# Optimization experiments

Measured on AMD Instinct MI355X. Metric: run time of the kernel, lower is better.

## Reference

```python
import jax, jax.numpy as jnp
import numpy as np

B, DIM, HH, WW = 8, 512, 64, 64
HEADS, DH = 8, 64
INNER = HEADS * DH
EPS = 1e-5  # ChanLayerNorm2D eps


def _chan_norm(x, g, b):
    # channel-wise layernorm over axis 1 (biased variance, like torch.var(unbiased=False))
    m = jnp.mean(x, axis=1, keepdims=True)
    v = jnp.mean((x - m) ** 2, axis=1, keepdims=True)
    return (x - m) / jnp.sqrt(v + EPS) * g + b


def _l2norm(x):
    # F.normalize(dim=1), eps=1e-12
    n = jnp.sqrt(jnp.sum(x * x, axis=1, keepdims=True))
    return x / jnp.maximum(n, 1e-12)


def setup_inputs() -> dict:
    key = jax.random.key(0)
    ks = jax.random.split(key, 10)
    sc = 1.0 / np.sqrt(DIM)
    return {
        "context": jax.random.normal(ks[0], (B, DIM, HH, WW), jnp.float32),
        "query_source": jax.random.normal(ks[1], (B, DIM, HH, WW), jnp.float32),
        "ctx_g": jnp.ones((1, DIM, 1, 1), jnp.float32),
        "ctx_b": jnp.zeros((1, DIM, 1, 1), jnp.float32),
        "qs_g": jnp.ones((1, DIM, 1, 1), jnp.float32),
        "qs_b": jnp.zeros((1, DIM, 1, 1), jnp.float32),
        "w_q": jax.random.normal(ks[2], (INNER, DIM), jnp.float32) * sc,
        "w_kv": jax.random.normal(ks[3], (2 * INNER, DIM), jnp.float32) * sc,
        "w_out": jax.random.normal(ks[4], (DIM, INNER), jnp.float32) * (1.0 / np.sqrt(INNER)),
        "gamma": jax.random.normal(ks[5], (1,), jnp.float32) * 0.5,
    }


def reference(context, query_source, ctx_g, ctx_b, qs_g, qs_b, w_q, w_kv, w_out, gamma):
    b, c, height, width = query_source.shape
    kh = int(height ** 0.5)  # default height_top_k
    kw = int(width ** 0.5)   # default width_top_k

    ctx = _chan_norm(context, ctx_g, ctx_b)
    qs = _chan_norm(query_source, qs_g, qs_b)

    # 1x1 convs as GEMMs
    kv = jnp.einsum('oi,bihw->bohw', w_kv, ctx)
    k, v = jnp.split(kv, 2, axis=1)
    q = jnp.einsum('oi,bihw->bohw', w_q, qs)

    def fold(t):  # b (h c) H W -> (b h) c H W
        return t.reshape(b, HEADS, DH, height, width).reshape(b * HEADS, DH, height, width)

    q, k, v = fold(q), fold(k), fold(v)
    q, k = _l2norm(q), _l2norm(k)

    # dual pruning (kh < height and kw < width here)
    q_abs = jnp.abs(q)
    k_abs = jnp.abs(k)
    q_probe = jnp.sum(q_abs, axis=(2, 3))            # (bh, c)

    # height selection
    k_height = jnp.sum(k_abs, axis=3)                # (bh, c, H)
    score_r = jnp.einsum('bc,bch->bh', q_probe, k_height)
    _, idx_h = jax.lax.top_k(score_r, kh)            # (bh, kh)
    k = jnp.take_along_axis(k, idx_h[:, None, :, None], axis=2)
    v = jnp.take_along_axis(v, idx_h[:, None, :, None], axis=2)

    # width selection (scores use pre-height-gather k_abs, as in original)
    k_width = jnp.sum(k_abs, axis=2)                 # (bh, c, W)
    score_c = jnp.einsum('bc,bcw->bw', q_probe, k_width)
    _, idx_w = jax.lax.top_k(score_c, kw)            # (bh, kw)
    k = jnp.take_along_axis(k, idx_w[:, None, None, :], axis=3)
    v = jnp.take_along_axis(v, idx_w[:, None, None, :], axis=3)

    def flat(t):  # (bh) d h w -> (bh) (h w) d
        bh, d, h_, w_ = t.shape
        return t.transpose(0, 2, 3, 1).reshape(bh, h_ * w_, d)

    qf, kf, vf = flat(q), flat(k), flat(v)
    attn = jax.nn.softmax(jnp.einsum('bid,bjd->bij', qf, kf), axis=-1)
    out = jnp.einsum('bij,bjd->bid', attn, vf)       # (bh, H*W, d)

    out = out.reshape(b, HEADS, height, width, DH).transpose(0, 1, 4, 2, 3)
    out = out.reshape(b, INNER, height, width)
    out = jnp.einsum('oi,bihw->bohw', w_out, out)
    return gamma[0] * out + qs
```

## Files before the change

kernel.cpp:

```cpp
#include <hip/hip_runtime.h>
#include <math.h>

#define HW 4096
#define DIM 512

typedef __attribute__((ext_vector_type(8))) short short8;
typedef __attribute__((ext_vector_type(4))) float f32x4;

__device__ inline unsigned short f2bf(float f) {
    unsigned int u = __float_as_uint(f);
    u += 0x7fff + ((u >> 16) & 1);
    return (unsigned short)(u >> 16);
}
__device__ inline float bf2f(unsigned short h) {
    return __uint_as_float(((unsigned int)h) << 16);
}
__device__ inline unsigned pack2(float a, float b) {
    return (unsigned)f2bf(a) | ((unsigned)f2bf(b) << 16);
}

__device__ inline void gld16(const void* g, void* lds) {
    __builtin_amdgcn_global_load_lds(
        (const __attribute__((address_space(1))) unsigned int*)g,
        (__attribute__((address_space(3))) unsigned int*)lds, 16, 0, 0);
}

__global__ void prep_weights(const float* __restrict__ w_q, const float* __restrict__ w_kv,
                             const float* __restrict__ w_out,
                             const float* __restrict__ ctx_g, const float* __restrict__ ctx_b,
                             const float* __restrict__ qs_g, const float* __restrict__ qs_b,
                             unsigned short* __restrict__ wq_b, unsigned short* __restrict__ wk_b,
                             unsigned short* __restrict__ wo_b, float* __restrict__ wv_g,
                             float* __restrict__ Avec, float* __restrict__ Cvec)
{
    int blk = blockIdx.x;
    int widx = blk >> 9;
    int o = blk & 511;
    int tid = threadIdx.x;
    const float *src, *g = nullptr, *beta = nullptr;
    if (widx == 0)      { src = w_q  + (size_t)o * DIM; g = qs_g;  beta = qs_b; }
    else if (widx == 1) { src = w_kv + (size_t)o * DIM; g = ctx_g; beta = ctx_b; }
    else if (widx == 2) { src = w_kv + (size_t)(512 + o) * DIM; g = ctx_g; beta = ctx_b; }
    else                { src = w_out + (size_t)o * DIM; }
    float a = 0.f, c = 0.f;
    for (int i = tid; i < DIM; i += 256) {
        float w = src[i];
        if (widx == 3) { wo_b[(size_t)o * DIM + i] = f2bf(w); continue; }
        float wg = w * g[i];
        if (widx == 0)      wq_b[(size_t)o * DIM + i] = f2bf(wg);
        else if (widx == 1) wk_b[(size_t)o * DIM + i] = f2bf(wg);
        else                wv_g[(size_t)o * DIM + i] = wg;
        a += wg; c += w * beta[i];
    }
    if (widx == 3) return;
    __shared__ float sa[256], sc[256];
    sa[tid] = a; sc[tid] = c;
    __syncthreads();
    for (int s = 128; s > 0; s >>= 1) {
        if (tid < s) { sa[tid] += sa[tid + s]; sc[tid] += sc[tid + s]; }
        __syncthreads();
    }
    if (tid == 0) { Avec[widx * 512 + o] = sa[0]; Cvec[widx * 512 + o] = sc[0]; }
}

__global__ __launch_bounds__(256) void conv_stats(
    const float* __restrict__ ctx, const float* __restrict__ qs,
    unsigned short* __restrict__ ctx_t, unsigned short* __restrict__ qs_t,
    float* __restrict__ ctx_m, float* __restrict__ ctx_r,
    float* __restrict__ qs_m, float* __restrict__ qs_r)
{
    int which = blockIdx.z;
    int b = blockIdx.y;
    int p0 = blockIdx.x * 64;
    const float* X = (which ? qs : ctx) + (size_t)b * DIM * HW;
    unsigned short* Xt = (which ? qs_t : ctx_t) + (size_t)b * HW * DIM;
    int tid = threadIdx.x;
    int p = tid & 63;
    int q4 = tid >> 6;
    const float* col = X + p0 + p;

    __shared__ uint4 tile[64 * 32];
    __shared__ float sbuf[256], ssbuf[256];

    float s = 0.f, ss = 0.f;
    for (int chunk = 0; chunk < 2; chunk++) {
        for (int si = 0; si < 8; si++) {
            int cgl = q4 * 8 + si;
            int c = chunk * 256 + cgl * 8;
            float v[8];
#pragma unroll
            for (int j = 0; j < 8; j++) {
                v[j] = col[(size_t)(c + j) * HW];
                s += v[j]; ss = fmaf(v[j], v[j], ss);
            }
            uint4 pk;
            pk.x = pack2(v[0], v[1]);
            pk.y = pack2(v[2], v[3]);
            pk.z = pack2(v[4], v[5]);
            pk.w = pack2(v[6], v[7]);
            tile[p * 32 + (cgl ^ (p & 15))] = pk;
        }
        __syncthreads();
        int pr = tid >> 2, c2 = tid & 3;
        unsigned short* orow = Xt + (size_t)(p0 + pr) * 512 + chunk * 256;
#pragma unroll
        for (int si = 0; si < 8; si++) {
            int cgl = c2 + si * 4;
            uint4 d = tile[pr * 32 + (cgl ^ (pr & 15))];
            *(uint4*)(orow + cgl * 8) = d;
        }
        __syncthreads();
    }

    sbuf[tid] = s; ssbuf[tid] = ss;
    __syncthreads();
    if (tid < 64) {
        float st  = sbuf[tid] + sbuf[tid + 64] + sbuf[tid + 128] + sbuf[tid + 192];
        float sst = ssbuf[tid] + ssbuf[tid + 64] + ssbuf[tid + 128] + ssbuf[tid + 192];
        float m = st * (1.0f / DIM);
        float var = sst * (1.0f / DIM) - m * m;
        float r = 1.0f / sqrtf(var + 1e-5f);
        int pix = b * HW + p0 + tid;
        if (which == 0) { ctx_m[pix] = m; ctx_r[pix] = r; }
        else            { qs_m[pix]  = m; qs_r[pix]  = r; }
    }
}

template<int MODE>
__global__ __launch_bounds__(256) void gemm_mfma(
    const unsigned short* __restrict__ Wb, const unsigned short* __restrict__ Xt,
    float* __restrict__ Y, unsigned short* __restrict__ Ybf,
    const float* __restrict__ mean, const float* __restrict__ rstd,
    const float* __restrict__ Arow, const float* __restrict__ Crow,
    float* __restrict__ probe,
    const float* __restrict__ qsrc, const float* __restrict__ g,
    const float* __restrict__ beta, const float* __restrict__ gammaPtr)
{
    int b = blockIdx.z;
    int n0 = blockIdx.x * 128;
    int m0 = blockIdx.y * 128;
    const unsigned short* Xb = Xt + (size_t)b * HW * DIM;
    __shared__ uint4 AsBuf[512];
    __shared__ uint4 BsBuf[512];
    unsigned short* As = (unsigned short*)AsBuf;
    unsigned short* Bs = (unsigned short*)BsBuf;
    int tid = threadIdx.x;
    int lane = tid & 63;
    int wave = tid >> 6;
    int wbase = tid & 192;
    int wm = (wave >> 1) * 64;
    int wn = (wave & 1) * 64;
    int quad = lane >> 4;
    int l16 = lane & 15;

    int r0 = tid >> 2, c0 = (tid & 3) * 8;
    const unsigned short* pA0 = Wb + (size_t)(m0 + r0) * DIM + c0;
    const unsigned short* pA1 = Wb + (size_t)(m0 + 64 + r0) * DIM + c0;
    const unsigned short* pB0 = Xb + (size_t)(n0 + r0) * DIM + c0;
    const unsigned short* pB1 = Xb + (size_t)(n0 + 64 + r0) * DIM + c0;

    f32x4 acc[4][4];
#pragma unroll
    for (int i = 0; i < 4; i++)
#pragma unroll
        for (int j = 0; j < 4; j++) acc[i][j] = (f32x4){0.f, 0.f, 0.f, 0.f};

    for (int kt = 0; kt < 16; kt++) {
        gld16(pA0, AsBuf + wbase);
        gld16(pA1, AsBuf + 256 + wbase);
        gld16(pB0, BsBuf + wbase);
        gld16(pB1, BsBuf + 256 + wbase);
        pA0 += 32; pA1 += 32; pB0 += 32; pB1 += 32;
        __syncthreads();
        short8 af[4], bfr[4];
#pragma unroll
        for (int i = 0; i < 4; i++)
            af[i] = *(const short8*)(As + (wm + i * 16 + l16) * 32 + quad * 8);
#pragma unroll
        for (int j = 0; j < 4; j++)
            bfr[j] = *(const short8*)(Bs + (wn + j * 16 + l16) * 32 + quad * 8);
#pragma unroll
        for (int i = 0; i < 4; i++)
#pragma unroll
            for (int j = 0; j < 4; j++)
                acc[i][j] = __builtin_amdgcn_mfma_f32_16x16x32_bf16(af[i], bfr[j], acc[i][j], 0, 0, 0);
        __syncthreads();
    }

    if (MODE < 2) {
        float pa[4][4] = {};
#pragma unroll
        for (int j = 0; j < 4; j++) {
            int n = n0 + wn + j * 16 + l16;
            int pix = b * HW + n;
            float mn = mean[pix], rs = rstd[pix];
            float y[4][4];
            float s2 = 0.f;
#pragma unroll
            for (int i = 0; i < 4; i++) {
                int mb = m0 + wm + i * 16 + quad * 4;
#pragma unroll
                for (int r = 0; r < 4; r++) {
                    float v = rs * (acc[i][j][r] - mn * Arow[mb + r]) + Crow[mb + r];
                    y[i][r] = v;
                    s2 = fmaf(v, v, s2);
                }
            }
            s2 += __shfl_xor(s2, 16, 64);
            s2 += __shfl_xor(s2, 32, 64);
            float inv = 1.0f / fmaxf(sqrtf(s2), 1e-12f);
            unsigned short* orow = Ybf + (size_t)(b * HW + n) * 512 + m0 + wm + quad * 4;
#pragma unroll
            for (int i = 0; i < 4; i++) {
                float v0 = y[i][0] * inv, v1 = y[i][1] * inv;
                float v2 = y[i][2] * inv, v3 = y[i][3] * inv;
                uint2 pk; pk.x = pack2(v0, v1); pk.y = pack2(v2, v3);
                *(uint2*)(orow + i * 16) = pk;
                pa[i][0] += fabsf(v0); pa[i][1] += fabsf(v1);
                pa[i][2] += fabsf(v2); pa[i][3] += fabsf(v3);
            }
        }
#pragma unroll
        for (int i = 0; i < 4; i++)
#pragma unroll
            for (int r = 0; r < 4; r++) {
                float v = pa[i][r];
                v += __shfl_xor(v, 1, 64);
                v += __shfl_xor(v, 2, 64);
                v += __shfl_xor(v, 4, 64);
                v += __shfl_xor(v, 8, 64);
                pa[i][r] = v;
            }
        if (l16 == 0) {
#pragma unroll
            for (int i = 0; i < 4; i++)
#pragma unroll
                for (int r = 0; r < 4; r++) {
                    int m = m0 + wm + i * 16 + quad * 4 + r;
                    if (MODE == 0) atomicAdd(&probe[b * 512 + m], pa[i][r]);
                    else atomicAdd(&probe[(size_t)(b * 512 + m) * 64 + ((n0 + wn) >> 6)], pa[i][r]);
                }
        }
    } else {
        float* Yb = Y + (size_t)b * DIM * HW;
        float gamma = gammaPtr[0];
        const float* qb = qsrc + (size_t)b * DIM * HW;
#pragma unroll
        for (int j = 0; j < 4; j++) {
            int n = n0 + wn + j * 16 + l16;
            int pix = b * HW + n;
            float mn = mean[pix], rs = rstd[pix];
#pragma unroll
            for (int i = 0; i < 4; i++) {
                int mb = m0 + wm + i * 16 + quad * 4;
#pragma unroll
                for (int r = 0; r < 4; r++) {
                    int m = mb + r;
                    float qn = (qb[(size_t)m * HW + n] - mn) * rs * g[m] + beta[m];
                    Yb[(size_t)m * HW + n] = gamma * acc[i][j][r] + qn;
                }
            }
        }
    }
}

__global__ __launch_bounds__(256) void kws_kernel(const unsigned short* __restrict__ kbf,
                                                  float* __restrict__ kws)
{
    int blk = blockIdx.x;
    int b = blk >> 6, w = blk & 63;
    int tid = threadIdx.x;
    int c8 = tid & 63;
    int hq = tid >> 6;
    float a[8] = {};
    for (int hh = 0; hh < 16; hh++) {
        const unsigned short* row = kbf + ((size_t)(b * HW + (hq * 16 + hh) * 64 + w)) * 512 + c8 * 8;
        uint4 pk = *(const uint4*)row;
        const unsigned short* u = (const unsigned short*)&pk;
#pragma unroll
        for (int j = 0; j < 8; j++) a[j] += fabsf(bf2f(u[j]));
    }
    __shared__ float red[512 * 4];
#pragma unroll
    for (int j = 0; j < 8; j++) red[(c8 * 8 + j) * 4 + hq] = a[j];
    __syncthreads();
    if (tid < 256) {
        int c = tid;
        float v0 = red[c * 4] + red[c * 4 + 1] + red[c * 4 + 2] + red[c * 4 + 3];
        int c2 = tid + 256;
        float v1 = red[c2 * 4] + red[c2 * 4 + 1] + red[c2 * 4 + 2] + red[c2 * 4 + 3];
        kws[(size_t)(b * 512 + c) * 64 + w] = v0;
        kws[(size_t)(b * 512 + c2) * 64 + w] = v1;
    }
}

__global__ void score_topk(const float* __restrict__ qp, const float* __restrict__ khs,
                           const float* __restrict__ kws, int* __restrict__ idx_h, int* __restrict__ idx_w)
{
    int bh = blockIdx.x;
    int lane = threadIdx.x;
    float sr = 0.f, sc = 0.f;
    for (int c = 0; c < 64; c++) {
        float q = qp[bh * 64 + c];
        sr = fmaf(q, khs[(size_t)(bh * 64 + c) * 64 + lane], sr);
        sc = fmaf(q, kws[(size_t)(bh * 64 + c) * 64 + lane], sc);
    }
    float v = sr;
    for (int it = 0; it < 8; it++) {
        float bv = v; int bi = lane;
        for (int off = 1; off < 64; off <<= 1) {
            float ov = __shfl_xor(bv, off, 64);
            int oi = __shfl_xor(bi, off, 64);
            if (ov > bv || (ov == bv && oi < bi)) { bv = ov; bi = oi; }
        }
        if (lane == 0) idx_h[bh * 8 + it] = bi;
        if (lane == bi) v = -INFINITY;
    }
    v = sc;
    for (int it = 0; it < 8; it++) {
        float bv = v; int bi = lane;
        for (int off = 1; off < 64; off <<= 1) {
            float ov = __shfl_xor(bv, off, 64);
            int oi = __shfl_xor(bi, off, 64);
            if (ov > bv || (ov == bv && oi < bi)) { bv = ov; bi = oi; }
        }
        if (lane == 0) idx_w[bh * 8 + it] = bi;
        if (lane == bi) v = -INFINITY;
    }
}

__global__ void gather_kv(const unsigned short* __restrict__ kbf, const unsigned short* __restrict__ ctx_t,
                          const float* __restrict__ wv_g, const float* __restrict__ Av, const float* __restrict__ Cv,
                          const float* __restrict__ ctx_m, const float* __restrict__ ctx_r,
                          const int* __restrict__ idx_h, const int* __restrict__ idx_w,
                          unsigned short* __restrict__ kg, unsigned short* __restrict__ vgt)
{
    int blk = blockIdx.x;
    int bh = blk >> 6, j = blk & 63;
    int h = idx_h[bh * 8 + (j >> 3)];
    int w = idx_w[bh * 8 + (j & 7)];
    int p = h * 64 + w;
    int b = bh >> 3, head = bh & 7;
    int d = threadIdx.x;
    kg[(size_t)blk * 64 + d] = kbf[(size_t)(b * HW + p) * 512 + head * 64 + d];
    __shared__ float cx[DIM];
    const unsigned short* crow = ctx_t + (size_t)(b * HW + p) * 512;
    short8 cv = ((const short8*)crow)[d];
#pragma unroll
    for (int u = 0; u < 8; u++) cx[d * 8 + u] = bf2f((unsigned short)cv[u]);
    __syncthreads();
    int o = head * 64 + d;
    const float* wrow = wv_g + (size_t)o * DIM;
    float acc = 0.f;
    for (int i = 0; i < DIM; i++) acc = fmaf(wrow[i], cx[i], acc);
    int pix = b * HW + p;
    float v = ctx_r[pix] * (acc - ctx_m[pix] * Av[o]) + Cv[o];
    vgt[((size_t)bh * 64 + d) * 64 + j] = f2bf(v);
}

#define PROW 72
__global__ __launch_bounds__(256) void attn_mfma(
    const unsigned short* __restrict__ qbf, const unsigned short* __restrict__ kg,
    const unsigned short* __restrict__ vgt, unsigned short* __restrict__ abuf)
{
    int bh = blockIdx.y;
    int b = bh >> 3, head = bh & 7;
    int tid = threadIdx.x;
    int lane = tid & 63, wave = tid >> 6;
    int g = lane >> 4, l16 = lane & 15;
    int p0 = blockIdx.x * 256 + wave * 64;

    __shared__ unsigned short Plds[4][64 * PROW];
    unsigned short* P = Plds[wave];

    const unsigned short* kgb = kg + (size_t)bh * 4096;
    const unsigned short* vtb = vgt + (size_t)bh * 4096;
    const unsigned short* qb = qbf + (size_t)(b * HW) * 512 + head * 64;

    short8 Qf[4][2];
#pragma unroll
    for (int j = 0; j < 4; j++)
#pragma unroll
        for (int t = 0; t < 2; t++)
            Qf[j][t] = *(const short8*)(qb + (size_t)(p0 + j * 16 + l16) * 512 + t * 32 + g * 8);

    f32x4 S[4][4];
#pragma unroll
    for (int i = 0; i < 4; i++)
#pragma unroll
        for (int j = 0; j < 4; j++) S[i][j] = (f32x4){0.f, 0.f, 0.f, 0.f};
#pragma unroll
    for (int t = 0; t < 2; t++) {
        short8 Kf[4];
#pragma unroll
        for (int i = 0; i < 4; i++)
            Kf[i] = *(const short8*)(kgb + (i * 16 + l16) * 64 + t * 32 + g * 8);
#pragma unroll
        for (int i = 0; i < 4; i++)
#pragma unroll
            for (int j = 0; j < 4; j++)
                S[i][j] = __builtin_amdgcn_mfma_f32_16x16x32_bf16(Kf[i], Qf[j][t], S[i][j], 0, 0, 0);
    }

    float inv[4];
#pragma unroll
    for (int j = 0; j < 4; j++) {
        float e[4][4];
        float s = 0.f;
#pragma unroll
        for (int i = 0; i < 4; i++)
#pragma unroll
            for (int r = 0; r < 4; r++) { e[i][r] = __expf(S[i][j][r]); s += e[i][r]; }
        s += __shfl_xor(s, 16, 64);
        s += __shfl_xor(s, 32, 64);
        inv[j] = 1.0f / s;
        int row = j * 16 + l16;
#pragma unroll
        for (int i = 0; i < 4; i++) {
            uint2 pk;
            pk.x = pack2(e[i][0], e[i][1]);
            pk.y = pack2(e[i][2], e[i][3]);
            *(uint2*)(P + row * PROW + i * 16 + g * 4) = pk;
        }
    }

    f32x4 O[4][4];
#pragma unroll
    for (int i = 0; i < 4; i++)
#pragma unroll
        for (int j = 0; j < 4; j++) O[i][j] = (f32x4){0.f, 0.f, 0.f, 0.f};
#pragma unroll
    for (int t = 0; t < 2; t++) {
        short8 Vf[4], Pf[4];
#pragma unroll
        for (int i = 0; i < 4; i++)
            Vf[i] = *(const short8*)(vtb + (i * 16 + l16) * 64 + t * 32 + g * 8);
#pragma unroll
        for (int j = 0; j < 4; j++)
            Pf[j] = *(const short8*)(P + (j * 16 + l16) * PROW + t * 32 + g * 8);
#pragma unroll
        for (int i = 0; i < 4; i++)
#pragma unroll
            for (int j = 0; j < 4; j++)
                O[i][j] = __builtin_amdgcn_mfma_f32_16x16x32_bf16(Vf[i], Pf[j], O[i][j], 0, 0, 0);
    }

    unsigned short* ob = abuf + (size_t)(b * HW) * 512 + head * 64;
#pragma unroll
    for (int j = 0; j < 4; j++) {
        int p = p0 + j * 16 + l16;
#pragma unroll
        for (int i = 0; i < 4; i++) {
            uint2 pk;
            pk.x = pack2(O[i][j][0] * inv[j], O[i][j][1] * inv[j]);
            pk.y = pack2(O[i][j][2] * inv[j], O[i][j][3] * inv[j]);
            *(uint2*)(ob + (size_t)p * 512 + i * 16 + g * 4) = pk;
        }
    }
}

extern "C" void kernel_launch(void* const* d_in, const int* in_sizes, int n_in,
                              void* d_out, int out_size, void* d_ws, size_t ws_size,
                              hipStream_t stream)
{
    (void)in_sizes; (void)n_in; (void)out_size; (void)ws_size;
    const float* ctx   = (const float*)d_in[0];
    const float* qs    = (const float*)d_in[1];
    const float* ctx_g = (const float*)d_in[2];
    const float* ctx_b = (const float*)d_in[3];
    const float* qs_g  = (const float*)d_in[4];
    const float* qs_b  = (const float*)d_in[5];
    const float* w_q   = (const float*)d_in[6];
    const float* w_kv  = (const float*)d_in[7];
    const float* w_out = (const float*)d_in[8];
    const float* gamma = (const float*)d_in[9];
    float* out = (float*)d_out;

    char* base = (char*)d_ws;
    unsigned short* ctx_t = (unsigned short*)base;
    unsigned short* abuf  = ctx_t;
    unsigned short* qs_t  = (unsigned short*)(base + ((size_t)32 << 20));
    unsigned short* kbf   = qs_t;
    unsigned short* qbf   = (unsigned short*)(base + ((size_t)64 << 20));
    char* tail = base + ((size_t)96 << 20);
    unsigned short* wq_b = (unsigned short*)tail;
    unsigned short* wk_b = wq_b + 262144;
    unsigned short* wo_b = wk_b + 262144;
    float* wv_g  = (float*)(wo_b + 262144);
    float* Avec  = wv_g + 262144;
    float* Cvec  = Avec + 1536;
    float* ctx_m = Cvec + 1536;
    float* ctx_r = ctx_m + 32768;
    float* qs_m  = ctx_r + 32768;
    float* qs_r  = qs_m + 32768;
    float* qp    = qs_r + 32768;
    float* khs   = qp + 4096;
    float* kws   = khs + 262144;
    int*   idxh  = (int*)(kws + 262144);
    int*   idxw  = idxh + 512;
    unsigned short* kg  = (unsigned short*)(idxw + 512);
    unsigned short* vgt = kg + 262144;

    hipMemsetAsync(qp, 0, 4096 * sizeof(float), stream);
    hipMemsetAsync(khs, 0, 262144 * sizeof(float), stream);

    prep_weights<<<2048, 256, 0, stream>>>(w_q, w_kv, w_out, ctx_g, ctx_b, qs_g, qs_b,
                                           wq_b, wk_b, wo_b, wv_g, Avec, Cvec);
    conv_stats<<<dim3(64, 8, 2), 256, 0, stream>>>(ctx, qs, ctx_t, qs_t,
                                                   ctx_m, ctx_r, qs_m, qs_r);
    gemm_mfma<0><<<dim3(32, 4, 8), 256, 0, stream>>>(wq_b, qs_t, nullptr, qbf, qs_m, qs_r,
                                                     Avec, Cvec, qp, nullptr, nullptr, nullptr, nullptr);
    gemm_mfma<1><<<dim3(32, 4, 8), 256, 0, stream>>>(wk_b, ctx_t, nullptr, kbf, ctx_m, ctx_r,
                                                     Avec + 512, Cvec + 512, khs, nullptr, nullptr, nullptr, nullptr);
    kws_kernel<<<512, 256, 0, stream>>>(kbf, kws);
    score_topk<<<64, 64, 0, stream>>>(qp, khs, kws, idxh, idxw);
    gather_kv<<<4096, 64, 0, stream>>>(kbf, ctx_t, wv_g, Avec + 1024, Cvec + 1024,
                                       ctx_m, ctx_r, idxh, idxw, kg, vgt);
    attn_mfma<<<dim3(16, 64), 256, 0, stream>>>(qbf, kg, vgt, abuf);
    gemm_mfma<2><<<dim3(32, 4, 8), 256, 0, stream>>>(wo_b, abuf, out, nullptr, qs_m, qs_r,
                                                     nullptr, nullptr, nullptr, qs, qs_g, qs_b, gamma);
}
```

Measured before the change: 450.5 us.

## Split conv_stats across channel slices with atomic stat accumulation

The transpose-and-stats kernel now tiles over 32-channel by 512-pixel blocks, giving 2048 blocks instead of 1024. It loads float4 rows coalesced along pixels and transposes through a padded LDS tile into the bf16 channel-last layout. Per-pixel sum and sum-of-squares are accumulated across channel slices with global atomics, and a new finalize kernel turns them into mean and rstd. This aims to improve load coalescing and parallelism on a memory-bound pass, at the cost of an extra memset, an extra launch, and atomic traffic.

```diff
diff --git a/kernel.cpp b/kernel.cpp
--- a/kernel.cpp
+++ b/kernel.cpp
@@ -66,64 +66,96 @@
 __global__ __launch_bounds__(256) void conv_stats(
     const float* __restrict__ ctx, const float* __restrict__ qs,
     unsigned short* __restrict__ ctx_t, unsigned short* __restrict__ qs_t,
-    float* __restrict__ ctx_m, float* __restrict__ ctx_r,
-    float* __restrict__ qs_m, float* __restrict__ qs_r)
-{
-    int which = blockIdx.z;
-    int b = blockIdx.y;
-    int p0 = blockIdx.x * 64;
+    float* __restrict__ Sacc, float* __restrict__ Qacc)
+{
+    int id = blockIdx.x;
+    int pstrip = id & 7;
+    int cs = (id >> 3) & 15;
+    int b = (id >> 7) & 7;
+    int which = id >> 10;
+
     const float* X = (which ? qs : ctx) + (size_t)b * DIM * HW;
     unsigned short* Xt = (which ? qs_t : ctx_t) + (size_t)b * HW * DIM;
     int tid = threadIdx.x;
-    int p = tid & 63;
-    int q4 = tid >> 6;
-    const float* col = X + p0 + p;
-
-    __shared__ uint4 tile[64 * 32];
-    __shared__ float sbuf[256], ssbuf[256];
-
-    float s = 0.f, ss = 0.f;
-    for (int chunk = 0; chunk < 2; chunk++) {
-        for (int si = 0; si < 8; si++) {
-            int cgl = q4 * 8 + si;
-            int c = chunk * 256 + cgl * 8;
-            float v[8];
-#pragma unroll
-            for (int j = 0; j < 8; j++) {
-                v[j] = col[(size_t)(c + j) * HW];
-                s += v[j]; ss = fmaf(v[j], v[j], ss);
-            }
-            uint4 pk;
-            pk.x = pack2(v[0], v[1]);
-            pk.y = pack2(v[2], v[3]);
-            pk.z = pack2(v[4], v[5]);
-            pk.w = pack2(v[6], v[7]);
-            tile[p * 32 + (cgl ^ (p & 15))] = pk;
-        }
-        __syncthreads();
-        int pr = tid >> 2, c2 = tid & 3;
-        unsigned short* orow = Xt + (size_t)(p0 + pr) * 512 + chunk * 256;
-#pragma unroll
-        for (int si = 0; si < 8; si++) {
-            int cgl = c2 + si * 4;
-            uint4 d = tile[pr * 32 + (cgl ^ (pr & 15))];
-            *(uint4*)(orow + cgl * 8) = d;
-        }
-        __syncthreads();
-    }
-
-    sbuf[tid] = s; ssbuf[tid] = ss;
+    int p0 = pstrip * 512;
+    int c0 = cs * 32;
+
+    __shared__ unsigned short tile[32 * 514];
+    __shared__ float4 sT[128], qT[128];
+
+    int par = tid >> 7;
+    int t7 = tid & 127;
+    int pxl = t7 * 4;
+    const float* src = X + (size_t)(c0 + par) * HW + p0 + pxl;
+
+    float4 s4 = {0.f, 0.f, 0.f, 0.f};
+    float4 q4 = {0.f, 0.f, 0.f, 0.f};
+
+#pragma unroll
+    for (int i = 0; i < 16; i++) {
+        int c = 2 * i + par;
+        float4 v = *(const float4*)(src + (size_t)(2 * i) * HW);
+        s4.x += v.x; s4.y += v.y; s4.z += v.z; s4.w += v.w;
+        q4.x = fmaf(v.x, v.x, q4.x);
+        q4.y = fmaf(v.y, v.y, q4.y);
+        q4.z = fmaf(v.z, v.z, q4.z);
+        q4.w = fmaf(v.w, v.w, q4.w);
+        uint2 pk;
+        pk.x = pack2(v.x, v.y);
+        pk.y = pack2(v.z, v.w);
+        *(uint2*)(tile + c * 514 + pxl) = pk;
+    }
+
+    if (par) { sT[t7] = s4; qT[t7] = q4; }
     __syncthreads();
-    if (tid < 64) {
-        float st  = sbuf[tid] + sbuf[tid + 64] + sbuf[tid + 128] + sbuf[tid + 192];
-        float sst = ssbuf[tid] + ssbuf[tid + 64] + ssbuf[tid + 128] + ssbuf[tid + 192];
-        float m = st * (1.0f / DIM);
-        float var = sst * (1.0f / DIM) - m * m;
-        float r = 1.0f / sqrtf(var + 1e-5f);
-        int pix = b * HW + p0 + tid;
-        if (which == 0) { ctx_m[pix] = m; ctx_r[pix] = r; }
-        else            { qs_m[pix]  = m; qs_r[pix]  = r; }
-    }
+    if (!par) {
+        float4 o = sT[t7];
+        s4.x += o.x; s4.y += o.y; s4.z += o.z; s4.w += o.w;
+        o = qT[t7];
+        q4.x += o.x; q4.y += o.y; q4.z += o.z; q4.w += o.w;
+        int slot = which * 32768 + b * 4096 + p0 + pxl;
+        atomicAdd(&Sacc[slot + 0], s4.x);
+        atomicAdd(&Sacc[slot + 1], s4.y);
+        atomicAdd(&Sacc[slot + 2], s4.z);
+        atomicAdd(&Sacc[slot + 3], s4.w);
+        atomicAdd(&Qacc[slot + 0], q4.x);
+        atomicAdd(&Qacc[slot + 1], q4.y);
+        atomicAdd(&Qacc[slot + 2], q4.z);
+        atomicAdd(&Qacc[slot + 3], q4.w);
+    }
+
+    int cg = tid & 3;
+    int pxw = tid >> 2;
+#pragma unroll
+    for (int r = 0; r < 8; r++) {
+        int px = pxw + 64 * r;
+        const unsigned short* tr = tile + cg * 8 * 514 + px;
+        unsigned short u0 = tr[0 * 514], u1 = tr[1 * 514];
+        unsigned short u2 = tr[2 * 514], u3 = tr[3 * 514];
+        unsigned short u4 = tr[4 * 514], u5 = tr[5 * 514];
+        unsigned short u6 = tr[6 * 514], u7 = tr[7 * 514];
+        uint4 o;
+        o.x = (unsigned)u0 | ((unsigned)u1 << 16);
+        o.y = (unsigned)u2 | ((unsigned)u3 << 16);
+        o.z = (unsigned)u4 | ((unsigned)u5 << 16);
+        o.w = (unsigned)u6 | ((unsigned)u7 << 16);
+        *(uint4*)(Xt + (size_t)(p0 + px) * 512 + c0 + cg * 8) = o;
+    }
+}
+
+__global__ __launch_bounds__(256) void finalize_stats(
+    const float* __restrict__ Sacc, const float* __restrict__ Qacc,
+    float* __restrict__ ctx_m, float* __restrict__ ctx_r,
+    float* __restrict__ qs_m, float* __restrict__ qs_r)
+{
+    int i = blockIdx.x * 256 + threadIdx.x;
+    float s = Sacc[i], q = Qacc[i];
+    float m = s * (1.0f / DIM);
+    float var = q * (1.0f / DIM) - m * m;
+    float r = 1.0f / sqrtf(var + 1e-5f);
+    int pix = i & 32767;
+    if (i < 32768) { ctx_m[pix] = m; ctx_r[pix] = r; }
+    else           { qs_m[pix]  = m; qs_r[pix]  = r; }
 }
 
 template<int MODE>
@@ -500,14 +532,17 @@
     int*   idxw  = idxh + 512;
     unsigned short* kg  = (unsigned short*)(idxw + 512);
     unsigned short* vgt = kg + 262144;
+    float* Sacc = (float*)(vgt + 262144);
+    float* Qacc = Sacc + 65536;
 
     hipMemsetAsync(qp, 0, 4096 * sizeof(float), stream);
     hipMemsetAsync(khs, 0, 262144 * sizeof(float), stream);
+    hipMemsetAsync(Sacc, 0, 131072 * sizeof(float), stream);
 
     prep_weights<<<2048, 256, 0, stream>>>(w_q, w_kv, w_out, ctx_g, ctx_b, qs_g, qs_b,
                                            wq_b, wk_b, wo_b, wv_g, Avec, Cvec);
-    conv_stats<<<dim3(64, 8, 2), 256, 0, stream>>>(ctx, qs, ctx_t, qs_t,
-                                                   ctx_m, ctx_r, qs_m, qs_r);
+    conv_stats<<<2048, 256, 0, stream>>>(ctx, qs, ctx_t, qs_t, Sacc, Qacc);
+    finalize_stats<<<256, 256, 0, stream>>>(Sacc, Qacc, ctx_m, ctx_r, qs_m, qs_r);
     gemm_mfma<0><<<dim3(32, 4, 8), 256, 0, stream>>>(wq_b, qs_t, nullptr, qbf, qs_m, qs_r,
                                                      Avec, Cvec, qp, nullptr, nullptr, nullptr, nullptr);
     gemm_mfma<1><<<dim3(32, 4, 8), 256, 0, stream>>>(wk_b, ctx_t, nullptr, kbf, ctx_m, ctx_r,
```

Result: slower. 460.5 us (+2.2%).
